# Optimization experiments

Measured on AMD Instinct MI355X. Metric: run time of the kernel, lower is better.

## Reference

```python
import jax, jax.numpy as jnp
import numpy as np

N_NODES = 100000
N_EDGES = 3200000
EPS = 1e-12


def gcn_conv(x, W, b, src, dst, n_nodes):
    """PyG-style GCNConv: h = D^-1/2 (A+I) D^-1/2 X W + b (symmetric norm, self-loops)."""
    h = x @ W  # [N, out]
    # in-degree on destination nodes, plus 1 for the self loop
    deg = jnp.zeros((n_nodes,), h.dtype).at[dst].add(1.0) + 1.0
    dinv = jax.lax.rsqrt(deg)  # deg >= 1 so safe
    coef = dinv[src] * dinv[dst]  # per-edge norm
    agg = jax.ops.segment_sum(h[src] * coef[:, None], dst, num_segments=n_nodes)
    # self-loop contribution: norm = dinv[i]^2
    return agg + h * (dinv * dinv)[:, None] + b


def setup_inputs() -> dict:
    key = jax.random.key(0)
    ks = jax.random.split(key, 6)
    x = jax.random.normal(ks[0], (N_NODES, 64), jnp.float32)
    edge_index = jax.random.randint(ks[1], (2, N_EDGES), 0, N_NODES, jnp.int32)
    W1 = jax.random.normal(ks[2], (64, 128), jnp.float32) * (1.0 / np.sqrt(64))
    b1 = jnp.zeros((128,), jnp.float32)
    W2 = jax.random.normal(ks[3], (128, 64), jnp.float32) * (1.0 / np.sqrt(128))
    b2 = jnp.zeros((64,), jnp.float32)
    Wd = jax.random.normal(ks[4], (64, 256), jnp.float32) * (1.0 / np.sqrt(64))
    bd = jnp.zeros((256,), jnp.float32)
    return {"x": x, "edge_index": edge_index, "W1": W1, "b1": b1,
            "W2": W2, "b2": b2, "Wd": Wd, "bd": bd}


def reference(x, edge_index, W1, b1, W2, b2, Wd, bd):
    src, dst = edge_index[0], edge_index[1]
    n = x.shape[0]
    h = gcn_conv(x, W1, b1, src, dst, n)
    h = jax.nn.relu(h)
    # dropout is identity in eval mode
    h2 = gcn_conv(h, W2, b2, src, dst, n)
    norm = jnp.linalg.norm(h2, axis=1, keepdims=True)
    final_embeddings = h2 / (norm + EPS)
    logits = final_embeddings @ Wd + bd
    return jax.nn.log_softmax(logits, axis=-1), final_embeddings
```

## Files before the change

kernel.cpp:

```cpp
#include <hip/hip_runtime.h>
#include <math.h>

#define BIN_SHIFT 8
#define BIN_MAXB 512
#define BIN_CHUNK 8192

typedef __attribute__((ext_vector_type(8))) short bf16x8;
typedef __attribute__((ext_vector_type(4))) float f32x4;

__device__ __forceinline__ float bf2f(unsigned short u) {
    union { unsigned int i; float f; } v;
    v.i = ((unsigned int)u) << 16;
    return v.f;
}
__device__ __forceinline__ unsigned short f2bf(float f) {
    union { float f; unsigned int i; } v;
    v.f = f;
    unsigned int r = v.i + 0x7FFF + ((v.i >> 16) & 1);
    return (unsigned short)(r >> 16);
}
__device__ __forceinline__ float lo_bf(unsigned int u) {
    union { unsigned int i; float f; } v;
    v.i = u << 16;
    return v.f;
}
__device__ __forceinline__ float hi_bf(unsigned int u) {
    union { unsigned int i; float f; } v;
    v.i = u & 0xFFFF0000u;
    return v.f;
}

__global__ __launch_bounds__(256) void k_ccount(const int* __restrict__ dst, int E,
                                                int* __restrict__ ccounts) {
    __shared__ int hist[BIN_MAXB];
    int t = threadIdx.x;
    int e0 = blockIdx.x * BIN_CHUNK;
    int eEnd = e0 + BIN_CHUNK;
    if (eEnd > E) eEnd = E;
    for (int i = t; i < BIN_MAXB; i += 256) hist[i] = 0;
    __syncthreads();
    for (int e = e0 + t; e < eEnd; e += 256)
        atomicAdd(&hist[dst[e] >> BIN_SHIFT], 1);
    __syncthreads();
    for (int i = t; i < BIN_MAXB; i += 256) {
        int h = hist[i];
        if (h > 0) atomicAdd(&ccounts[i], h);
    }
}

__global__ void k_cscan(const int* __restrict__ ccounts, int NB, int N,
                        int* __restrict__ coff, int* __restrict__ ccur,
                        int* __restrict__ offsets) {
    __shared__ int s[BIN_MAXB];
    int t = threadIdx.x;
    int v = (t < NB) ? ccounts[t] : 0;
    s[t] = v;
    __syncthreads();
    for (int off = 1; off < BIN_MAXB; off <<= 1) {
        int tmp = (t >= off) ? s[t - off] : 0;
        __syncthreads();
        s[t] += tmp;
        __syncthreads();
    }
    int excl = s[t] - v;
    if (t < NB) {
        coff[t] = excl;
        ccur[t] = excl;
    }
    if (t == NB - 1) {
        coff[NB] = s[t];
        offsets[N] = s[t];
    }
}

__global__ __launch_bounds__(256) void k_binA(const int* __restrict__ src,
                                              const int* __restrict__ dst, int E,
                                              int* __restrict__ ccur,
                                              unsigned int* __restrict__ pairs) {
    __shared__ int hist[BIN_MAXB];
    __shared__ int base[BIN_MAXB];
    int t = threadIdx.x;
    int e0 = blockIdx.x * BIN_CHUNK;
    int eEnd = e0 + BIN_CHUNK;
    if (eEnd > E) eEnd = E;
    for (int i = t; i < BIN_MAXB; i += 256) hist[i] = 0;
    __syncthreads();
    for (int e = e0 + t; e < eEnd; e += 256) {
        int d = dst[e];
        atomicAdd(&hist[d >> BIN_SHIFT], 1);
    }
    __syncthreads();
    for (int i = t; i < BIN_MAXB; i += 256) {
        int h = hist[i];
        base[i] = (h > 0) ? atomicAdd(&ccur[i], h) : 0;
        hist[i] = 0;
    }
    __syncthreads();
    for (int e = e0 + t; e < eEnd; e += 256) {
        int d = dst[e];
        int s = src[e];
        int b = d >> BIN_SHIFT;
        int lp = atomicAdd(&hist[b], 1);
        pairs[base[b] + lp] = ((unsigned int)s << BIN_SHIFT) | (unsigned int)(d & 255);
    }
}

__global__ __launch_bounds__(256) void k_binfine(const unsigned int* __restrict__ pairs,
                                                 const int* __restrict__ coff,
                                                 int N,
                                                 int* __restrict__ counts,
                                                 int* __restrict__ offsets,
                                                 int* __restrict__ sorted_src) {
    __shared__ int hist[256];
    __shared__ int scan[256];
    __shared__ int lcur[256];
    int b = blockIdx.x;
    int t = threadIdx.x;
    int beg = coff[b], end = coff[b + 1];
    int dbase = b << BIN_SHIFT;
    hist[t] = 0;
    __syncthreads();
    for (int e = beg + t; e < end; e += 256)
        atomicAdd(&hist[pairs[e] & 255u], 1);
    __syncthreads();
    int v = hist[t];
    scan[t] = v;
    __syncthreads();
    for (int off = 1; off < 256; off <<= 1) {
        int tmp = (t >= off) ? scan[t - off] : 0;
        __syncthreads();
        scan[t] += tmp;
        __syncthreads();
    }
    int excl = scan[t] - v;
    int node = dbase + t;
    if (node < N) {
        counts[node] = v;
        offsets[node] = beg + excl;
    }
    lcur[t] = beg + excl;
    __syncthreads();
    for (int e = beg + t; e < end; e += 256) {
        unsigned int pk = pairs[e];
        int pos = atomicAdd(&lcur[pk & 255u], 1);
        sorted_src[pos] = (int)(pk >> BIN_SHIFT);
    }
}

__global__ void k_dinv(const int* __restrict__ counts, int N, float* __restrict__ dinv) {
    int i = blockIdx.x * blockDim.x + threadIdx.x;
    if (i < N) dinv[i] = rsqrtf((float)counts[i] + 1.0f);
}

__global__ void k_prep(const float* __restrict__ x, const float* __restrict__ dinv,
                       int N, unsigned short* __restrict__ xsc) {
    int i = blockIdx.x * blockDim.x + threadIdx.x;
    if (i >= N * 16) return;
    int node = i >> 4;
    float d = dinv[node];
    float4 v = ((const float4*)x)[i];
    ushort4 u;
    u.x = f2bf(v.x * d);
    u.y = f2bf(v.y * d);
    u.z = f2bf(v.z * d);
    u.w = f2bf(v.w * d);
    ((ushort4*)xsc)[i] = u;
}

template <bool FINAL>
__global__ __launch_bounds__(256) void k_agg_bf(const unsigned short* __restrict__ fsc,
                                                const float* __restrict__ dinv,
                                                const int* __restrict__ offsets,
                                                const int* __restrict__ sorted_src,
                                                const float* __restrict__ b2,
                                                int N, float* __restrict__ out,
                                                unsigned short* __restrict__ fbf) {
    int wid = threadIdx.x >> 6;
    int lane = threadIdx.x & 63;
    int g = lane >> 3;
    int c = lane & 7;
    int i = blockIdx.x * 4 + wid;
    if (i >= N) return;
    int beg = offsets[i], end = offsets[i + 1];
    const unsigned short* fsc_c = fsc + (c << 3);

    float a0 = 0.f, a1 = 0.f, a2 = 0.f, a3 = 0.f;
    float a4 = 0.f, a5 = 0.f, a6 = 0.f, a7 = 0.f;

    int e = beg;
    for (; e + 15 < end; e += 16) {
        int s0 = sorted_src[e + g];
        int s1 = sorted_src[e + 8 + g];
        uint4 v0 = *(const uint4*)(fsc_c + ((unsigned)s0 << 6));
        uint4 v1 = *(const uint4*)(fsc_c + ((unsigned)s1 << 6));
        a0 += lo_bf(v0.x); a1 += hi_bf(v0.x);
        a2 += lo_bf(v0.y); a3 += hi_bf(v0.y);
        a4 += lo_bf(v0.z); a5 += hi_bf(v0.z);
        a6 += lo_bf(v0.w); a7 += hi_bf(v0.w);
        a0 += lo_bf(v1.x); a1 += hi_bf(v1.x);
        a2 += lo_bf(v1.y); a3 += hi_bf(v1.y);
        a4 += lo_bf(v1.z); a5 += hi_bf(v1.z);
        a6 += lo_bf(v1.w); a7 += hi_bf(v1.w);
    }
    for (; e + 7 < end; e += 8) {
        int s0 = sorted_src[e + g];
        uint4 v0 = *(const uint4*)(fsc_c + ((unsigned)s0 << 6));
        a0 += lo_bf(v0.x); a1 += hi_bf(v0.x);
        a2 += lo_bf(v0.y); a3 += hi_bf(v0.y);
        a4 += lo_bf(v0.z); a5 += hi_bf(v0.z);
        a6 += lo_bf(v0.w); a7 += hi_bf(v0.w);
    }
    int rem = end - e;
    if (rem > 0) {
        int idx = e + ((g < rem) ? g : 0);
        int s0 = sorted_src[idx];
        uint4 v0 = *(const uint4*)(fsc_c + ((unsigned)s0 << 6));
        if (g < rem) {
            a0 += lo_bf(v0.x); a1 += hi_bf(v0.x);
            a2 += lo_bf(v0.y); a3 += hi_bf(v0.y);
            a4 += lo_bf(v0.z); a5 += hi_bf(v0.z);
            a6 += lo_bf(v0.w); a7 += hi_bf(v0.w);
        }
    }
#pragma unroll
    for (int m = 8; m <= 32; m <<= 1) {
        a0 += __shfl_xor(a0, m, 64);
        a1 += __shfl_xor(a1, m, 64);
        a2 += __shfl_xor(a2, m, 64);
        a3 += __shfl_xor(a3, m, 64);
        a4 += __shfl_xor(a4, m, 64);
        a5 += __shfl_xor(a5, m, 64);
        a6 += __shfl_xor(a6, m, 64);
        a7 += __shfl_xor(a7, m, 64);
    }
    {
        uint4 v = *(const uint4*)(fsc_c + ((unsigned)i << 6));
        a0 += lo_bf(v.x); a1 += hi_bf(v.x);
        a2 += lo_bf(v.y); a3 += hi_bf(v.y);
        a4 += lo_bf(v.z); a5 += hi_bf(v.z);
        a6 += lo_bf(v.w); a7 += hi_bf(v.w);
    }
    float di = dinv[i];
    if (!FINAL) {
        if (g == 0) {
            float* op = out + (size_t)i * 64 + (c << 3);
            *(float4*)(op + 0) = make_float4(a0 * di, a1 * di, a2 * di, a3 * di);
            *(float4*)(op + 4) = make_float4(a4 * di, a5 * di, a6 * di, a7 * di);
        }
    } else {
        const float* bp = b2 + (c << 3);
        float4 bA = *(const float4*)(bp + 0);
        float4 bB = *(const float4*)(bp + 4);
        float z0 = a0 * di + bA.x;
        float z1 = a1 * di + bA.y;
        float z2 = a2 * di + bA.z;
        float z3 = a3 * di + bA.w;
        float z4 = a4 * di + bB.x;
        float z5 = a5 * di + bB.y;
        float z6 = a6 * di + bB.z;
        float z7 = a7 * di + bB.w;
        float sq = z0 * z0 + z1 * z1 + z2 * z2 + z3 * z3 +
                   z4 * z4 + z5 * z5 + z6 * z6 + z7 * z7;
#pragma unroll
        for (int m = 1; m <= 4; m <<= 1) sq += __shfl_xor(sq, m, 64);
        float r = 1.0f / (sqrtf(sq) + 1e-12f);
        if (g == 0) {
            float* op = out + (size_t)i * 64 + (c << 3);
            *(float4*)(op + 0) = make_float4(z0 * r, z1 * r, z2 * r, z3 * r);
            *(float4*)(op + 4) = make_float4(z4 * r, z5 * r, z6 * r, z7 * r);
        } else if (g == 1) {
            uint4 pk;
            pk.x = (unsigned)f2bf(z0 * r) | ((unsigned)f2bf(z1 * r) << 16);
            pk.y = (unsigned)f2bf(z2 * r) | ((unsigned)f2bf(z3 * r) << 16);
            pk.z = (unsigned)f2bf(z4 * r) | ((unsigned)f2bf(z5 * r) << 16);
            pk.w = (unsigned)f2bf(z6 * r) | ((unsigned)f2bf(z7 * r) << 16);
            *(uint4*)(fbf + (size_t)i * 64 + (c << 3)) = pk;
        }
    }
}

__global__ __launch_bounds__(256) void k_fused(const float* __restrict__ z1,
                                               const float* __restrict__ W1,
                                               const float* __restrict__ b1,
                                               const float* __restrict__ W2,
                                               const float* __restrict__ dinv,
                                               int N, unsigned short* __restrict__ gsc) {
    __shared__ unsigned short W1s[64 * 128];
    __shared__ unsigned short W2s[128 * 64];
    __shared__ float As[32][68];
    __shared__ unsigned short Hs[32][132];
    __shared__ float b1s[128];
    __shared__ float dl[32];

    int t = threadIdx.x;
    int r0blk = blockIdx.x * 32;

    for (int idx = t; idx < 2048; idx += 256) {
        float4 v = ((const float4*)W1)[idx];
        ushort4 u;
        u.x = f2bf(v.x); u.y = f2bf(v.y); u.z = f2bf(v.z); u.w = f2bf(v.w);
        ((ushort4*)W1s)[idx] = u;
    }
    for (int idx = t; idx < 2048; idx += 256) {
        float4 v = ((const float4*)W2)[idx];
        ushort4 u;
        u.x = f2bf(v.x); u.y = f2bf(v.y); u.z = f2bf(v.z); u.w = f2bf(v.w);
        ((ushort4*)W2s)[idx] = u;
    }
    if (t < 128) b1s[t] = b1[t];
    for (int idx = t; idx < 512; idx += 256) {
        int r = idx >> 4;
        int c4 = idx & 15;
        int row = r0blk + r;
        float4 v = (row < N) ? ((const float4*)z1)[(size_t)row * 16 + c4]
                             : make_float4(0.f, 0.f, 0.f, 0.f);
        *(float4*)&As[r][c4 * 4] = v;
    }
    if (t < 32) dl[t] = (r0blk + t < N) ? dinv[r0blk + t] : 0.f;
    __syncthreads();

    int rg = t >> 5;
    int cg = t & 31;
    int r0 = rg * 4;
    int c0 = cg * 4;

    float acc[4][4];
#pragma unroll
    for (int j = 0; j < 4; j++)
#pragma unroll
        for (int q = 0; q < 4; q++) acc[j][q] = 0.f;
    for (int k = 0; k < 64; k++) {
        float a0 = As[r0 + 0][k];
        float a1 = As[r0 + 1][k];
        float a2 = As[r0 + 2][k];
        float a3 = As[r0 + 3][k];
        uint2 wu = *(const uint2*)&W1s[k * 128 + c0];
        float wx = lo_bf(wu.x), wy = hi_bf(wu.x);
        float wz = lo_bf(wu.y), ww = hi_bf(wu.y);
        acc[0][0] = fmaf(a0, wx, acc[0][0]); acc[0][1] = fmaf(a0, wy, acc[0][1]);
        acc[0][2] = fmaf(a0, wz, acc[0][2]); acc[0][3] = fmaf(a0, ww, acc[0][3]);
        acc[1][0] = fmaf(a1, wx, acc[1][0]); acc[1][1] = fmaf(a1, wy, acc[1][1]);
        acc[1][2] = fmaf(a1, wz, acc[1][2]); acc[1][3] = fmaf(a1, ww, acc[1][3]);
        acc[2][0] = fmaf(a2, wx, acc[2][0]); acc[2][1] = fmaf(a2, wy, acc[2][1]);
        acc[2][2] = fmaf(a2, wz, acc[2][2]); acc[2][3] = fmaf(a2, ww, acc[2][3]);
        acc[3][0] = fmaf(a3, wx, acc[3][0]); acc[3][1] = fmaf(a3, wy, acc[3][1]);
        acc[3][2] = fmaf(a3, wz, acc[3][2]); acc[3][3] = fmaf(a3, ww, acc[3][3]);
    }
#pragma unroll
    for (int j = 0; j < 4; j++) {
        ushort4 hu;
        hu.x = f2bf(fmaxf(acc[j][0] + b1s[c0 + 0], 0.f));
        hu.y = f2bf(fmaxf(acc[j][1] + b1s[c0 + 1], 0.f));
        hu.z = f2bf(fmaxf(acc[j][2] + b1s[c0 + 2], 0.f));
        hu.w = f2bf(fmaxf(acc[j][3] + b1s[c0 + 3], 0.f));
        *(ushort4*)&Hs[r0 + j][c0] = hu;
    }
    __syncthreads();

    float acc2[4][2];
#pragma unroll
    for (int j = 0; j < 4; j++) { acc2[j][0] = 0.f; acc2[j][1] = 0.f; }
    int c2 = cg * 2;
    for (int k = 0; k < 128; k += 2) {
        ushort2 au0 = *(const ushort2*)&Hs[r0 + 0][k];
        ushort2 au1 = *(const ushort2*)&Hs[r0 + 1][k];
        ushort2 au2 = *(const ushort2*)&Hs[r0 + 2][k];
        ushort2 au3 = *(const ushort2*)&Hs[r0 + 3][k];
        ushort2 w0u = *(const ushort2*)&W2s[k * 64 + c2];
        ushort2 w1u = *(const ushort2*)&W2s[(k + 1) * 64 + c2];
        float wx0 = bf2f(w0u.x), wy0 = bf2f(w0u.y);
        float wx1 = bf2f(w1u.x), wy1 = bf2f(w1u.y);
        float a00 = bf2f(au0.x), a01 = bf2f(au0.y);
        float a10 = bf2f(au1.x), a11 = bf2f(au1.y);
        float a20 = bf2f(au2.x), a21 = bf2f(au2.y);
        float a30 = bf2f(au3.x), a31 = bf2f(au3.y);
        acc2[0][0] = fmaf(a00, wx0, fmaf(a01, wx1, acc2[0][0]));
        acc2[0][1] = fmaf(a00, wy0, fmaf(a01, wy1, acc2[0][1]));
        acc2[1][0] = fmaf(a10, wx0, fmaf(a11, wx1, acc2[1][0]));
        acc2[1][1] = fmaf(a10, wy0, fmaf(a11, wy1, acc2[1][1]));
        acc2[2][0] = fmaf(a20, wx0, fmaf(a21, wx1, acc2[2][0]));
        acc2[2][1] = fmaf(a20, wy0, fmaf(a21, wy1, acc2[2][1]));
        acc2[3][0] = fmaf(a30, wx0, fmaf(a31, wx1, acc2[3][0]));
        acc2[3][1] = fmaf(a30, wy0, fmaf(a31, wy1, acc2[3][1]));
    }
#pragma unroll
    for (int j = 0; j < 4; j++) {
        int row = r0blk + r0 + j;
        if (row < N) {
            float d = dl[r0 + j];
            ushort2 o;
            o.x = f2bf(acc2[j][0] * d);
            o.y = f2bf(acc2[j][1] * d);
            *(ushort2*)&gsc[(size_t)row * 64 + c2] = o;
        }
    }
}

__global__ __launch_bounds__(256, 2) void k_dec(const unsigned short* __restrict__ Fbf,
                                                const float* __restrict__ Wd,
                                                const float* __restrict__ bd,
                                                int N, float* __restrict__ out) {
    __shared__ float redM[4][16];
    __shared__ float redS[4][16];
    int t = threadIdx.x;
    int w = t >> 6, lane = t & 63;
    int l15 = lane & 15, lhi = lane >> 4;
    int cbase = w * 64;

    bf16x8 B[4][2];
    float bb[4];
#pragma unroll
    for (int c = 0; c < 4; c++) {
        int col = cbase + c * 16 + l15;
        bb[c] = bd[col];
#pragma unroll
        for (int kh = 0; kh < 2; kh++) {
            bf16x8 bf;
#pragma unroll
            for (int j = 0; j < 8; j++) {
                int k = kh * 32 + lhi * 8 + j;
                bf[j] = (short)f2bf(Wd[k * 256 + col]);
            }
            B[c][kh] = bf;
        }
    }

    int nTasks = (N + 15) / 16;
    for (int task = blockIdx.x; task < nTasks; task += gridDim.x) {
        int r0 = task * 16;
        int rowA = r0 + l15;
        bf16x8 A0 = {};
        bf16x8 A1 = {};
        if (rowA < N) {
            A0 = *(const bf16x8*)(Fbf + (size_t)rowA * 64 + lhi * 8);
            A1 = *(const bf16x8*)(Fbf + (size_t)rowA * 64 + 32 + lhi * 8);
        }
        float z[4][4];
#pragma unroll
        for (int c = 0; c < 4; c++) {
            f32x4 acc = {0.f, 0.f, 0.f, 0.f};
            acc = __builtin_amdgcn_mfma_f32_16x16x32_bf16(A0, B[c][0], acc, 0, 0, 0);
            acc = __builtin_amdgcn_mfma_f32_16x16x32_bf16(A1, B[c][1], acc, 0, 0, 0);
#pragma unroll
            for (int r = 0; r < 4; r++) z[c][r] = acc[r] + bb[c];
        }
        float M[4];
#pragma unroll
        for (int r = 0; r < 4; r++) {
            float m = fmaxf(fmaxf(z[0][r], z[1][r]), fmaxf(z[2][r], z[3][r]));
#pragma unroll
            for (int mm = 1; mm <= 8; mm <<= 1) m = fmaxf(m, __shfl_xor(m, mm, 64));
            M[r] = m;
        }
        if (l15 == 0) {
#pragma unroll
            for (int r = 0; r < 4; r++) redM[w][lhi * 4 + r] = M[r];
        }
        __syncthreads();
        float sr[4];
#pragma unroll
        for (int r = 0; r < 4; r++) {
            int rl = lhi * 4 + r;
            M[r] = fmaxf(fmaxf(redM[0][rl], redM[1][rl]), fmaxf(redM[2][rl], redM[3][rl]));
            float s = __expf(z[0][r] - M[r]) + __expf(z[1][r] - M[r]) +
                      __expf(z[2][r] - M[r]) + __expf(z[3][r] - M[r]);
#pragma unroll
            for (int mm = 1; mm <= 8; mm <<= 1) s += __shfl_xor(s, mm, 64);
            sr[r] = s;
        }
        if (l15 == 0) {
#pragma unroll
            for (int r = 0; r < 4; r++) redS[w][lhi * 4 + r] = sr[r];
        }
        __syncthreads();
#pragma unroll
        for (int r = 0; r < 4; r++) {
            int rl = lhi * 4 + r;
            int grow = r0 + rl;
            if (grow < N) {
                float s = redS[0][rl] + redS[1][rl] + redS[2][rl] + redS[3][rl];
                float lz = M[r] + __logf(s);
#pragma unroll
                for (int c = 0; c < 4; c++)
                    out[(size_t)grow * 256 + cbase + c * 16 + l15] = z[c][r] - lz;
            }
        }
        __syncthreads();
    }
}

extern "C" void kernel_launch(void* const* d_in, const int* in_sizes, int n_in,
                              void* d_out, int out_size, void* d_ws, size_t ws_size,
                              hipStream_t stream) {
    const float* x = (const float*)d_in[0];
    const int* ei = (const int*)d_in[1];
    const float* W1 = (const float*)d_in[2];
    const float* b1 = (const float*)d_in[3];
    const float* W2 = (const float*)d_in[4];
    const float* b2 = (const float*)d_in[5];
    const float* Wd = (const float*)d_in[6];
    const float* bd = (const float*)d_in[7];
    int N = in_sizes[0] / 64;
    int E = in_sizes[1] / 2;
    const int* srcIdx = ei;
    const int* dstIdx = ei + E;
    int NB = (N + 255) >> BIN_SHIFT;

    char* w = (char*)d_ws;
    auto alloc = [&](size_t bytes) {
        void* p = (void*)w;
        w += (bytes + 255) & ~(size_t)255;
        return p;
    };
    int* counts = (int*)alloc((size_t)N * 4);
    int* offsets = (int*)alloc((size_t)(N + 1) * 4);
    int* ccounts = (int*)alloc((size_t)BIN_MAXB * 4);
    int* coff = (int*)alloc((size_t)(BIN_MAXB + 1) * 4);
    int* ccur = (int*)alloc((size_t)BIN_MAXB * 4);
    int* sorted_src = (int*)alloc((size_t)E * 4);
    float* dinv = (float*)alloc((size_t)N * 4);
    unsigned short* xsc = (unsigned short*)alloc((size_t)N * 64 * 2);
    unsigned short* gsc = (unsigned short*)alloc((size_t)N * 64 * 2);
    unsigned short* fbf = xsc;
    size_t z1_bytes = (size_t)N * 64 * 4;
    size_t pairs_bytes = (size_t)E * 4;
    float* z1 = (float*)alloc(z1_bytes > pairs_bytes ? z1_bytes : pairs_bytes);
    unsigned int* pairs = (unsigned int*)z1;
    float* outLogp = (float*)d_out;
    float* outFinal = (float*)d_out + (size_t)N * 256;

    hipMemsetAsync(ccounts, 0, (size_t)BIN_MAXB * 4, stream);

    k_ccount<<<(E + BIN_CHUNK - 1) / BIN_CHUNK, 256, 0, stream>>>(dstIdx, E, ccounts);
    k_cscan<<<1, BIN_MAXB, 0, stream>>>(ccounts, NB, N, coff, ccur, offsets);
    k_binA<<<(E + BIN_CHUNK - 1) / BIN_CHUNK, 256, 0, stream>>>(srcIdx, dstIdx, E, ccur, pairs);
    k_binfine<<<NB, 256, 0, stream>>>(pairs, coff, N, counts, offsets, sorted_src);

    k_dinv<<<(N + 255) / 256, 256, 0, stream>>>(counts, N, dinv);
    k_prep<<<(N * 16 + 255) / 256, 256, 0, stream>>>(x, dinv, N, xsc);

    k_agg_bf<false><<<(N + 3) / 4, 256, 0, stream>>>(xsc, dinv, offsets, sorted_src, nullptr, N, z1, nullptr);

    k_fused<<<(N + 31) / 32, 256, 0, stream>>>(z1, W1, b1, W2, dinv, N, gsc);

    k_agg_bf<true><<<(N + 3) / 4, 256, 0, stream>>>(gsc, dinv, offsets, sorted_src, b2, N, outFinal, fbf);

    k_dec<<<1024, 256, 0, stream>>>(fbf, Wd, bd, N, outLogp);
}
```

Measured before the change: 483.3 us.

## Rewrite fused two-layer transform with MFMA and bf16 intermediate

The fused X·W1→ReLU→·W2 kernel moves from scalar FMA loops with shared-memory weight tiles to bf16 MFMA instructions. Weights are held in registers per wave, and a persistent grid of 512 blocks processes 16-row tasks. The first aggregation now writes its output in bf16 instead of fp32, which halves that intermediate's write and read traffic. In exchange, per-wave weight fragments raise register pressure, and the extra bf16 rounding of the aggregated features adds numerical error.

Measured after the change: 421.2 us. 1.15x faster.

```diff
diff --git a/kernel.cpp b/kernel.cpp
--- a/kernel.cpp
+++ b/kernel.cpp
@@ -174,7 +174,7 @@
                                                 const int* __restrict__ sorted_src,
                                                 const float* __restrict__ b2,
                                                 int N, float* __restrict__ out,
-                                                unsigned short* __restrict__ fbf) {
+                                                unsigned short* __restrict__ outbf) {
     int wid = threadIdx.x >> 6;
     int lane = threadIdx.x & 63;
     int g = lane >> 3;
@@ -243,9 +243,12 @@
     float di = dinv[i];
     if (!FINAL) {
         if (g == 0) {
-            float* op = out + (size_t)i * 64 + (c << 3);
-            *(float4*)(op + 0) = make_float4(a0 * di, a1 * di, a2 * di, a3 * di);
-            *(float4*)(op + 4) = make_float4(a4 * di, a5 * di, a6 * di, a7 * di);
+            uint4 pk;
+            pk.x = (unsigned)f2bf(a0 * di) | ((unsigned)f2bf(a1 * di) << 16);
+            pk.y = (unsigned)f2bf(a2 * di) | ((unsigned)f2bf(a3 * di) << 16);
+            pk.z = (unsigned)f2bf(a4 * di) | ((unsigned)f2bf(a5 * di) << 16);
+            pk.w = (unsigned)f2bf(a6 * di) | ((unsigned)f2bf(a7 * di) << 16);
+            *(uint4*)(outbf + (size_t)i * 64 + (c << 3)) = pk;
         }
     } else {
         const float* bp = b2 + (c << 3);
@@ -274,124 +277,93 @@
             pk.y = (unsigned)f2bf(z2 * r) | ((unsigned)f2bf(z3 * r) << 16);
             pk.z = (unsigned)f2bf(z4 * r) | ((unsigned)f2bf(z5 * r) << 16);
             pk.w = (unsigned)f2bf(z6 * r) | ((unsigned)f2bf(z7 * r) << 16);
-            *(uint4*)(fbf + (size_t)i * 64 + (c << 3)) = pk;
-        }
-    }
-}
-
-__global__ __launch_bounds__(256) void k_fused(const float* __restrict__ z1,
-                                               const float* __restrict__ W1,
-                                               const float* __restrict__ b1,
-                                               const float* __restrict__ W2,
-                                               const float* __restrict__ dinv,
-                                               int N, unsigned short* __restrict__ gsc) {
-    __shared__ unsigned short W1s[64 * 128];
-    __shared__ unsigned short W2s[128 * 64];
-    __shared__ float As[32][68];
-    __shared__ unsigned short Hs[32][132];
-    __shared__ float b1s[128];
-    __shared__ float dl[32];
-
+            *(uint4*)(outbf + (size_t)i * 64 + (c << 3)) = pk;
+        }
+    }
+}
+
+__global__ __launch_bounds__(256, 2) void k_fused(const unsigned short* __restrict__ z1bf,
+                                                  const float* __restrict__ W1,
+                                                  const float* __restrict__ b1,
+                                                  const float* __restrict__ W2,
+                                                  const float* __restrict__ dinv,
+                                                  int N, unsigned short* __restrict__ gsc) {
+    __shared__ unsigned short Hlds[4][16][136];
     int t = threadIdx.x;
-    int r0blk = blockIdx.x * 32;
-
-    for (int idx = t; idx < 2048; idx += 256) {
-        float4 v = ((const float4*)W1)[idx];
-        ushort4 u;
-        u.x = f2bf(v.x); u.y = f2bf(v.y); u.z = f2bf(v.z); u.w = f2bf(v.w);
-        ((ushort4*)W1s)[idx] = u;
-    }
-    for (int idx = t; idx < 2048; idx += 256) {
-        float4 v = ((const float4*)W2)[idx];
-        ushort4 u;
-        u.x = f2bf(v.x); u.y = f2bf(v.y); u.z = f2bf(v.z); u.w = f2bf(v.w);
-        ((ushort4*)W2s)[idx] = u;
-    }
-    if (t < 128) b1s[t] = b1[t];
-    for (int idx = t; idx < 512; idx += 256) {
-        int r = idx >> 4;
-        int c4 = idx & 15;
-        int row = r0blk + r;
-        float4 v = (row < N) ? ((const float4*)z1)[(size_t)row * 16 + c4]
-                             : make_float4(0.f, 0.f, 0.f, 0.f);
-        *(float4*)&As[r][c4 * 4] = v;
-    }
-    if (t < 32) dl[t] = (r0blk + t < N) ? dinv[r0blk + t] : 0.f;
-    __syncthreads();
-
-    int rg = t >> 5;
-    int cg = t & 31;
-    int r0 = rg * 4;
-    int c0 = cg * 4;
-
-    float acc[4][4];
-#pragma unroll
-    for (int j = 0; j < 4; j++)
-#pragma unroll
-        for (int q = 0; q < 4; q++) acc[j][q] = 0.f;
-    for (int k = 0; k < 64; k++) {
-        float a0 = As[r0 + 0][k];
-        float a1 = As[r0 + 1][k];
-        float a2 = As[r0 + 2][k];
-        float a3 = As[r0 + 3][k];
-        uint2 wu = *(const uint2*)&W1s[k * 128 + c0];
-        float wx = lo_bf(wu.x), wy = hi_bf(wu.x);
-        float wz = lo_bf(wu.y), ww = hi_bf(wu.y);
-        acc[0][0] = fmaf(a0, wx, acc[0][0]); acc[0][1] = fmaf(a0, wy, acc[0][1]);
-        acc[0][2] = fmaf(a0, wz, acc[0][2]); acc[0][3] = fmaf(a0, ww, acc[0][3]);
-        acc[1][0] = fmaf(a1, wx, acc[1][0]); acc[1][1] = fmaf(a1, wy, acc[1][1]);
-        acc[1][2] = fmaf(a1, wz, acc[1][2]); acc[1][3] = fmaf(a1, ww, acc[1][3]);
-        acc[2][0] = fmaf(a2, wx, acc[2][0]); acc[2][1] = fmaf(a2, wy, acc[2][1]);
-        acc[2][2] = fmaf(a2, wz, acc[2][2]); acc[2][3] = fmaf(a2, ww, acc[2][3]);
-        acc[3][0] = fmaf(a3, wx, acc[3][0]); acc[3][1] = fmaf(a3, wy, acc[3][1]);
-        acc[3][2] = fmaf(a3, wz, acc[3][2]); acc[3][3] = fmaf(a3, ww, acc[3][3]);
-    }
-#pragma unroll
-    for (int j = 0; j < 4; j++) {
-        ushort4 hu;
-        hu.x = f2bf(fmaxf(acc[j][0] + b1s[c0 + 0], 0.f));
-        hu.y = f2bf(fmaxf(acc[j][1] + b1s[c0 + 1], 0.f));
-        hu.z = f2bf(fmaxf(acc[j][2] + b1s[c0 + 2], 0.f));
-        hu.w = f2bf(fmaxf(acc[j][3] + b1s[c0 + 3], 0.f));
-        *(ushort4*)&Hs[r0 + j][c0] = hu;
-    }
-    __syncthreads();
-
-    float acc2[4][2];
-#pragma unroll
-    for (int j = 0; j < 4; j++) { acc2[j][0] = 0.f; acc2[j][1] = 0.f; }
-    int c2 = cg * 2;
-    for (int k = 0; k < 128; k += 2) {
-        ushort2 au0 = *(const ushort2*)&Hs[r0 + 0][k];
-        ushort2 au1 = *(const ushort2*)&Hs[r0 + 1][k];
-        ushort2 au2 = *(const ushort2*)&Hs[r0 + 2][k];
-        ushort2 au3 = *(const ushort2*)&Hs[r0 + 3][k];
-        ushort2 w0u = *(const ushort2*)&W2s[k * 64 + c2];
-        ushort2 w1u = *(const ushort2*)&W2s[(k + 1) * 64 + c2];
-        float wx0 = bf2f(w0u.x), wy0 = bf2f(w0u.y);
-        float wx1 = bf2f(w1u.x), wy1 = bf2f(w1u.y);
-        float a00 = bf2f(au0.x), a01 = bf2f(au0.y);
-        float a10 = bf2f(au1.x), a11 = bf2f(au1.y);
-        float a20 = bf2f(au2.x), a21 = bf2f(au2.y);
-        float a30 = bf2f(au3.x), a31 = bf2f(au3.y);
-        acc2[0][0] = fmaf(a00, wx0, fmaf(a01, wx1, acc2[0][0]));
-        acc2[0][1] = fmaf(a00, wy0, fmaf(a01, wy1, acc2[0][1]));
-        acc2[1][0] = fmaf(a10, wx0, fmaf(a11, wx1, acc2[1][0]));
-        acc2[1][1] = fmaf(a10, wy0, fmaf(a11, wy1, acc2[1][1]));
-        acc2[2][0] = fmaf(a20, wx0, fmaf(a21, wx1, acc2[2][0]));
-        acc2[2][1] = fmaf(a20, wy0, fmaf(a21, wy1, acc2[2][1]));
-        acc2[3][0] = fmaf(a30, wx0, fmaf(a31, wx1, acc2[3][0]));
-        acc2[3][1] = fmaf(a30, wy0, fmaf(a31, wy1, acc2[3][1]));
-    }
-#pragma unroll
-    for (int j = 0; j < 4; j++) {
-        int row = r0blk + r0 + j;
-        if (row < N) {
-            float d = dl[r0 + j];
-            ushort2 o;
-            o.x = f2bf(acc2[j][0] * d);
-            o.y = f2bf(acc2[j][1] * d);
-            *(ushort2*)&gsc[(size_t)row * 64 + c2] = o;
+    int w = t >> 6, lane = t & 63;
+    int l15 = lane & 15, lhi = lane >> 4;
+
+    bf16x8 A1f[8][2];
+#pragma unroll
+    for (int ct = 0; ct < 8; ct++)
+#pragma unroll
+        for (int kh = 0; kh < 2; kh++) {
+            bf16x8 f;
+#pragma unroll
+            for (int j = 0; j < 8; j++)
+                f[j] = (short)f2bf(W1[(kh * 32 + lhi * 8 + j) * 128 + ct * 16 + l15]);
+            A1f[ct][kh] = f;
+        }
+    bf16x8 A2f[4][4];
+#pragma unroll
+    for (int ct2 = 0; ct2 < 4; ct2++)
+#pragma unroll
+        for (int kh2 = 0; kh2 < 4; kh2++) {
+            bf16x8 f;
+#pragma unroll
+            for (int j = 0; j < 8; j++)
+                f[j] = (short)f2bf(W2[(kh2 * 32 + lhi * 8 + j) * 64 + ct2 * 16 + l15]);
+            A2f[ct2][kh2] = f;
+        }
+    float b1v[8][4];
+#pragma unroll
+    for (int ct = 0; ct < 8; ct++) {
+        float4 bv = *(const float4*)&b1[ct * 16 + lhi * 4];
+        b1v[ct][0] = bv.x; b1v[ct][1] = bv.y; b1v[ct][2] = bv.z; b1v[ct][3] = bv.w;
+    }
+
+    int nTasks = (N + 15) / 16;
+    for (int task = blockIdx.x * 4 + w; task < nTasks; task += gridDim.x * 4) {
+        int r0 = task * 16;
+        int node = r0 + l15;
+        bf16x8 Bz0 = {};
+        bf16x8 Bz1 = {};
+        if (node < N) {
+            Bz0 = *(const bf16x8*)(z1bf + (size_t)node * 64 + lhi * 8);
+            Bz1 = *(const bf16x8*)(z1bf + (size_t)node * 64 + 32 + lhi * 8);
+        }
+#pragma unroll
+        for (int ct = 0; ct < 8; ct++) {
+            f32x4 acc = {0.f, 0.f, 0.f, 0.f};
+            acc = __builtin_amdgcn_mfma_f32_16x16x32_bf16(A1f[ct][0], Bz0, acc, 0, 0, 0);
+            acc = __builtin_amdgcn_mfma_f32_16x16x32_bf16(A1f[ct][1], Bz1, acc, 0, 0, 0);
+            ushort4 hu;
+            hu.x = f2bf(fmaxf(acc[0] + b1v[ct][0], 0.f));
+            hu.y = f2bf(fmaxf(acc[1] + b1v[ct][1], 0.f));
+            hu.z = f2bf(fmaxf(acc[2] + b1v[ct][2], 0.f));
+            hu.w = f2bf(fmaxf(acc[3] + b1v[ct][3], 0.f));
+            *(ushort4*)&Hlds[w][l15][ct * 16 + lhi * 4] = hu;
+        }
+        bf16x8 Bh[4];
+#pragma unroll
+        for (int kh2 = 0; kh2 < 4; kh2++)
+            Bh[kh2] = *(const bf16x8*)&Hlds[w][l15][kh2 * 32 + lhi * 8];
+        float di = (node < N) ? dinv[node] : 0.f;
+#pragma unroll
+        for (int ct2 = 0; ct2 < 4; ct2++) {
+            f32x4 acc = {0.f, 0.f, 0.f, 0.f};
+            acc = __builtin_amdgcn_mfma_f32_16x16x32_bf16(A2f[ct2][0], Bh[0], acc, 0, 0, 0);
+            acc = __builtin_amdgcn_mfma_f32_16x16x32_bf16(A2f[ct2][1], Bh[1], acc, 0, 0, 0);
+            acc = __builtin_amdgcn_mfma_f32_16x16x32_bf16(A2f[ct2][2], Bh[2], acc, 0, 0, 0);
+            acc = __builtin_amdgcn_mfma_f32_16x16x32_bf16(A2f[ct2][3], Bh[3], acc, 0, 0, 0);
+            if (node < N) {
+                ushort4 o;
+                o.x = f2bf(acc[0] * di);
+                o.y = f2bf(acc[1] * di);
+                o.z = f2bf(acc[2] * di);
+                o.w = f2bf(acc[3] * di);
+                *(ushort4*)(gsc + (size_t)node * 64 + ct2 * 16 + lhi * 4) = o;
+            }
         }
     }
 }
@@ -522,10 +494,10 @@
     unsigned short* xsc = (unsigned short*)alloc((size_t)N * 64 * 2);
     unsigned short* gsc = (unsigned short*)alloc((size_t)N * 64 * 2);
     unsigned short* fbf = xsc;
-    size_t z1_bytes = (size_t)N * 64 * 4;
+    size_t z1_bytes = (size_t)N * 64 * 2;
     size_t pairs_bytes = (size_t)E * 4;
-    float* z1 = (float*)alloc(z1_bytes > pairs_bytes ? z1_bytes : pairs_bytes);
-    unsigned int* pairs = (unsigned int*)z1;
+    unsigned short* z1bf = (unsigned short*)alloc(z1_bytes > pairs_bytes ? z1_bytes : pairs_bytes);
+    unsigned int* pairs = (unsigned int*)z1bf;
     float* outLogp = (float*)d_out;
     float* outFinal = (float*)d_out + (size_t)N * 256;
 
@@ -539,9 +511,9 @@
     k_dinv<<<(N + 255) / 256, 256, 0, stream>>>(counts, N, dinv);
     k_prep<<<(N * 16 + 255) / 256, 256, 0, stream>>>(x, dinv, N, xsc);
 
-    k_agg_bf<false><<<(N + 3) / 4, 256, 0, stream>>>(xsc, dinv, offsets, sorted_src, nullptr, N, z1, nullptr);
-
-    k_fused<<<(N + 31) / 32, 256, 0, stream>>>(z1, W1, b1, W2, dinv, N, gsc);
+    k_agg_bf<false><<<(N + 3) / 4, 256, 0, stream>>>(xsc, dinv, offsets, sorted_src, nullptr, N, nullptr, z1bf);
+
+    k_fused<<<512, 256, 0, stream>>>(z1bf, W1, b1, W2, dinv, N, gsc);
 
     k_agg_bf<true><<<(N + 3) / 4, 256, 0, stream>>>(gsc, dinv, offsets, sorted_src, b2, N, outFinal, fbf);
 
```
